# Optimization experiments

Measured on AMD Instinct MI355X. Metric: run time of the kernel, lower is better.

Reference implementation:

```python
import jax, jax.numpy as jnp
import numpy as np

B, C, H, W, K = 4, 64, 128, 128, 3
K2 = K * K
PAD = (K - 1) // 2  # same padding for 3x3


def setup_inputs() -> dict:
    key = jax.random.key(0)
    ks = jax.random.split(key, 9)
    s = 0.05
    return {
        "x": jax.random.normal(ks[0], (B, C, H, W), jnp.float32),
        "inter": jax.random.normal(ks[1], (B, C, H, W), jnp.float32),
        # offset/mask predictor conv: input cat([x, inter]) -> 3*K2 channels (dy, dx, mask)
        "w_offset": jax.random.normal(ks[2], (3 * K2, 2 * C, K, K), jnp.float32) * s,
        "b_offset": jnp.zeros((3 * K2,), jnp.float32),
        # deformable conv weight (bias=False per DGM init)
        "w_dcn": jax.random.normal(ks[3], (C, C, K, K), jnp.float32) * s,
        # SFT gamma branch: two 1x1 convs (bias=False)
        "w_g1": jax.random.normal(ks[4], (C, C), jnp.float32) * s,
        "w_g2": jax.random.normal(ks[5], (C, C), jnp.float32) * s,
        # SFT beta branch: two 1x1 convs (bias=False)
        "w_b1": jax.random.normal(ks[6], (C, C), jnp.float32) * s,
        "w_b2": jax.random.normal(ks[7], (C, C), jnp.float32) * s,
    }


def _lrelu(v):
    # LeakyReLU(0.1)
    return jnp.where(v >= 0, v, 0.1 * v)


def _conv(x, w, b=None):
    y = jax.lax.conv_general_dilated(
        x, w, window_strides=(1, 1), padding=[(PAD, PAD), (PAD, PAD)],
        dimension_numbers=("NCHW", "OIHW", "NCHW"))
    if b is not None:
        y = y + b[None, :, None, None]
    return y


def _bilinear_gather(x, py, px):
    """x: [B,C,H,W]; py, px: [B,K2,H,W] float sample coords.
    Returns samples [B,K2,H,W,C]; out-of-bounds treated as zero (DCN zero-pad)."""
    y0 = jnp.floor(py)
    x0 = jnp.floor(px)
    wy = (py - y0)[..., None]
    wx = (px - x0)[..., None]

    def gather(yi, xi):
        valid = ((yi >= 0) & (yi < H) & (xi >= 0) & (xi < W)).astype(x.dtype)
        yc = jnp.clip(yi, 0, H - 1).astype(jnp.int32)
        xc = jnp.clip(xi, 0, W - 1).astype(jnp.int32)
        bidx = jnp.arange(B)[:, None, None, None]
        v = x[bidx, :, yc, xc]  # advanced indexing -> [B,K2,H,W,C]
        return v * valid[..., None]

    v00 = gather(y0, x0)
    v01 = gather(y0, x0 + 1)
    v10 = gather(y0 + 1, x0)
    v11 = gather(y0 + 1, x0 + 1)
    return (v00 * (1 - wy) * (1 - wx) + v01 * (1 - wy) * wx
            + v10 * wy * (1 - wx) + v11 * wy * wx)


def _dgm_forward(x, inter, w_offset, b_offset, w_dcn, w_g1, w_g2, w_b1, w_b2):
    # --- WADCN branch: modulated deformable conv, offsets predicted from cat(x, inter)
    om = _conv(jnp.concatenate([x, inter], axis=1), w_offset, b_offset)  # [B,3K2,H,W]
    dy, dx, m = jnp.split(om, 3, axis=1)  # each [B,K2,H,W]
    mask = jax.nn.sigmoid(m)

    ky, kx = jnp.meshgrid(jnp.arange(K), jnp.arange(K), indexing="ij")
    ky = ky.reshape(K2).astype(x.dtype)
    kx = kx.reshape(K2).astype(x.dtype)
    hh = jnp.arange(H, dtype=x.dtype)
    ww = jnp.arange(W, dtype=x.dtype)
    # sample coords: base grid + kernel-tap offset + learned offset
    py = hh[None, None, :, None] + (ky - PAD)[None, :, None, None] + dy  # [B,K2,H,W]
    px = ww[None, None, None, :] + (kx - PAD)[None, :, None, None] + dx

    samp = _bilinear_gather(x, py, px) * mask[..., None]  # [B,K2,H,W,C]
    dcn_out = jnp.einsum("bkhwc,ock->bohw", samp, w_dcn.reshape(C, C, K2))

    # --- SFT branch: two 1x1-conv + LeakyReLU chains producing gamma/beta
    gamma = jnp.einsum("oc,bchw->bohw", w_g2,
                       _lrelu(jnp.einsum("oc,bchw->bohw", w_g1, inter)))
    beta = jnp.einsum("oc,bchw->bohw", w_b2,
                      _lrelu(jnp.einsum("oc,bchw->bohw", w_b1, inter)))
    sft_out = x * gamma + beta

    # --- fused residual combine (DGM.relu is defined but never applied)
    return x + dcn_out + sft_out


def reference(x, inter, w_offset, b_offset, w_dcn, w_g1, w_g2, w_b1, w_b2):
    return _dgm_forward(x, inter, w_offset, b_offset, w_dcn, w_g1, w_g2, w_b1, w_b2)
```

## Files before the change

kernel.cpp:

```cpp
#include <hip/hip_runtime.h>
#include <hip/hip_bf16.h>
#include <math.h>

#define BB 4
#define CC 64
#define HH 128
#define WW 128
#define HW (HH*WW)
#define NPIX (BB*HW)

typedef __attribute__((ext_vector_type(8))) short short8;
typedef __attribute__((ext_vector_type(4))) float f32x4;

__device__ __forceinline__ float bf2f(ushort u) {
  union { unsigned u; float f; } v; v.u = ((unsigned)u) << 16; return v.f;
}
__device__ __forceinline__ ushort f2bf(float f) {
  __hip_bfloat16 h = __float2bfloat16(f); return *(ushort*)&h;
}

__global__ __launch_bounds__(256) void k_prep(
    const float* __restrict__ x, const float* __restrict__ inter,
    const float* __restrict__ w_off, const float* __restrict__ w_dcn,
    const float* __restrict__ wg1, const float* __restrict__ wb1,
    const float* __restrict__ wg2, const float* __restrict__ wb2,
    ushort* __restrict__ x_clh, ushort* __restrict__ inter_clh,
    ushort* __restrict__ wfb, ushort* __restrict__ wdT,
    ushort* __restrict__ w1gb, ushort* __restrict__ w1bb,
    ushort* __restrict__ w2gb, ushort* __restrict__ w2bb,
    float* __restrict__ zp) {
  __shared__ __align__(16) float tile[64 * 128];
  int blk = blockIdx.x;
  int tid = threadIdx.x;
  if (blk < 1024) {
    int sel = blk >> 9;
    int bh = blk & 511;
    int b = bh >> 7, h = bh & 127;
    const float* src = sel ? inter : x;
    ushort* dst = sel ? inter_clh : x_clh;
    const float* sp = src + (size_t)(b * 64) * HW + h * WW;
#pragma unroll
    for (int it = 0; it < 8; ++it) {
      int idx = it * 256 + tid;
      int c = idx >> 5, wq = idx & 31;
      float4 v = *(const float4*)(sp + (size_t)c * HW + wq * 4);
      int s = (c >> 3) & 7;
      *(float4*)(&tile[c * 128 + ((wq ^ s) << 2)]) = v;
    }
    __syncthreads();
    ushort* dp = dst + ((size_t)b * HW + h * WW) * 64;
#pragma unroll
    for (int it = 0; it < 4; ++it) {
      int idx = it * 256 + tid;
      int w = idx >> 3, c8 = idx & 7;
      short8 outv;
#pragma unroll
      for (int j = 0; j < 8; ++j) {
        int c = c8 * 8 + j;
        int sl = (w >> 2) ^ c8;
        float f = tile[c * 128 + (sl << 2) + (w & 3)];
        outv[j] = (short)f2bf(f);
      }
      *(short8*)(dp + (size_t)w * 64 + c8 * 8) = outv;
    }
  } else if (blk < 1168) {
    int i = (blk - 1024) * 256 + tid;
    if (i < 64) zp[i] = 0.f;
    if (i < 9 * 32 * 128) {
      int tap = i >> 12, rem = i & 4095, m = rem >> 7, c = rem & 127;
      float v = (m < 27) ? w_off[(size_t)(m * 128 + c) * 9 + tap] : 0.f;
      wfb[i] = f2bf(v);
    }
  } else if (blk < 1312) {
    int i = (blk - 1168) * 256 + tid;
    if (i < 64 * 64 * 9) {
      int o = i / 576, rem = i % 576, k = rem >> 6, c = rem & 63;
      wdT[i] = f2bf(w_dcn[(o * 64 + c) * 9 + k]);
    }
  } else {
    int i = (blk - 1312) * 256 + tid;
    int m = i >> 12, j = i & 4095;
    const float* src = (m == 0) ? wg1 : (m == 1) ? wb1 : (m == 2) ? wg2 : wb2;
    ushort* dst = (m == 0) ? w1gb : (m == 1) ? w1bb : (m == 2) ? w2gb : w2bb;
    dst[j] = f2bf(src[j]);
  }
}

#define CPITCH 72
#define SPITCH 200
#define NPX 32
#define FPX 72

__global__ __launch_bounds__(256) void k_omega(
    const float* __restrict__ x, const ushort* __restrict__ x_clh,
    const ushort* __restrict__ inter_clh,
    const float* __restrict__ b_off, const ushort* __restrict__ wfb,
    const ushort* __restrict__ wdT,
    const ushort* __restrict__ w1gb, const ushort* __restrict__ w1bb,
    const ushort* __restrict__ w2gb, const ushort* __restrict__ w2bb,
    const ushort* __restrict__ zp16, float* __restrict__ out) {
  __shared__ __align__(16) ushort BIGB[6 * 34 * CPITCH];
  ushort* S  = BIGB;
  ushort* Sg = BIGB + 6400;
  ushort* Sb = Sg + NPX * FPX;
  int*   cy  = (int*)(BIGB + 6400);
  int*   cx  = cy + 288;
  float* cwy = (float*)(cx + 288);
  float* cwx = cwy + 288;
  float* cm  = cwx + 288;
  float* oml = (float*)(BIGB + 11008);

  int tid = threadIdx.x;
  int wave = tid >> 6, lane = tid & 63;
  int quad = lane >> 4, col = lane & 15;
  int rr = lane >> 3, g = lane & 7;
  int pg0 = blockIdx.x * NPX;
  int b = pg0 >> 14, hw0 = pg0 & 16383;
  int h = hw0 >> 7, w0 = hw0 & 127;
  int pt = wave >> 1, mt = wave & 1;
  int o_base = __builtin_amdgcn_readfirstlane(wave * 16);

  {
    int ch = (tid & 7) * 8;
    unsigned bbase = (unsigned)b * HW;
#pragma unroll
    for (int it = 0; it < 7; ++it) {
      int e = it * 32 + (tid >> 3);
      if (e < 204) {
        int srcrow = e / 34, pxl = e % 34;
        int src = srcrow / 3, row = srcrow % 3;
        int hs = h + row - 1;
        int ps = w0 + pxl - 1;
        bool ok = ((unsigned)hs < 128u) && ((unsigned)ps < 128u);
        int hc = hs < 0 ? 0 : (hs > 127 ? 127 : hs);
        int pc = ps < 0 ? 0 : (ps > 127 ? 127 : ps);
        const ushort* sb = src ? inter_clh : x_clh;
        short8 v = *(const short8*)(sb + ((size_t)(bbase + (hc << 7) + pc)) * 64 + ch);
        short8 z = {0, 0, 0, 0, 0, 0, 0, 0};
        if (!ok) v = z;
        *(short8*)(&BIGB[e * CPITCH + ch]) = v;
      }
    }
  }
  __syncthreads();

  f32x4 accx = {0.f, 0.f, 0.f, 0.f}, acci = {0.f, 0.f, 0.f, 0.f};
  {
    const ushort* wb0 = wfb + (size_t)(mt * 16 + col) * 128 + quad * 8;
    int pxb = pt * 16 + col;
#pragma unroll
    for (int ky = 0; ky < 3; ++ky) {
#pragma unroll
      for (int kx = 0; kx < 3; ++kx) {
        int tap = ky * 3 + kx;
        const ushort* wt = wb0 + (size_t)tap * 4096;
#pragma unroll
        for (int ks = 0; ks < 2; ++ks) {
          short8 a0 = *(const short8*)(wt + ks * 32);
          short8 b0 = *(const short8*)(&BIGB[(ky * 34 + pxb + kx) * CPITCH + ks * 32 + quad * 8]);
          accx = __builtin_amdgcn_mfma_f32_16x16x32_bf16(a0, b0, accx, 0, 0, 0);
          short8 a1 = *(const short8*)(wt + 64 + ks * 32);
          short8 b1 = *(const short8*)(&BIGB[((3 + ky) * 34 + pxb + kx) * CPITCH + ks * 32 + quad * 8]);
          acci = __builtin_amdgcn_mfma_f32_16x16x32_bf16(a1, b1, acci, 0, 0, 0);
        }
      }
    }
  }
  __syncthreads();

#pragma unroll
  for (int r = 0; r < 4; ++r) {
    int o = mt * 16 + quad * 4 + r;
    if (o < 27) oml[o * 33 + pt * 16 + col] = accx[r] + acci[r];
  }

  f32x4 ag[2], ab[2];
#pragma unroll
  for (int nt = 0; nt < 2; ++nt) {
    ag[nt] = (f32x4){0.f, 0.f, 0.f, 0.f};
    ab[nt] = (f32x4){0.f, 0.f, 0.f, 0.f};
  }
#pragma unroll
  for (int ks = 0; ks < 2; ++ks) {
    short8 a_g = *(const short8*)(w1gb + (size_t)(o_base + col) * 64 + ks * 32 + quad * 8);
    short8 a_b = *(const short8*)(w1bb + (size_t)(o_base + col) * 64 + ks * 32 + quad * 8);
#pragma unroll
    for (int nt = 0; nt < 2; ++nt) {
      short8 bf = *(const short8*)(inter_clh + (size_t)(pg0 + nt * 16 + col) * 64 + ks * 32 + quad * 8);
      ag[nt] = __builtin_amdgcn_mfma_f32_16x16x32_bf16(a_g, bf, ag[nt], 0, 0, 0);
      ab[nt] = __builtin_amdgcn_mfma_f32_16x16x32_bf16(a_b, bf, ab[nt], 0, 0, 0);
    }
  }
#pragma unroll
  for (int nt = 0; nt < 2; ++nt) {
    int px = nt * 16 + col;
    ushort pkg[4], pkb[4];
#pragma unroll
    for (int r = 0; r < 4; ++r) {
      float vg = ag[nt][r]; vg = vg >= 0.f ? vg : 0.1f * vg;
      float vb = ab[nt][r]; vb = vb >= 0.f ? vb : 0.1f * vb;
      pkg[r] = f2bf(vg); pkb[r] = f2bf(vb);
    }
    *(uint2*)(&Sg[px * FPX + o_base + quad * 4]) = *(uint2*)pkg;
    *(uint2*)(&Sb[px * FPX + o_base + quad * 4]) = *(uint2*)pkb;
  }
  __syncthreads();

  f32x4 gg[2], gb[2];
#pragma unroll
  for (int nt = 0; nt < 2; ++nt) {
    gg[nt] = (f32x4){0.f, 0.f, 0.f, 0.f};
    gb[nt] = (f32x4){0.f, 0.f, 0.f, 0.f};
  }
#pragma unroll
  for (int ks = 0; ks < 2; ++ks) {
    short8 a_g = *(const short8*)(w2gb + (size_t)(o_base + col) * 64 + ks * 32 + quad * 8);
    short8 a_b = *(const short8*)(w2bb + (size_t)(o_base + col) * 64 + ks * 32 + quad * 8);
#pragma unroll
    for (int nt = 0; nt < 2; ++nt) {
      short8 bgf = *(const short8*)(Sg + (nt * 16 + col) * FPX + ks * 32 + quad * 8);
      short8 bbf = *(const short8*)(Sb + (nt * 16 + col) * FPX + ks * 32 + quad * 8);
      gg[nt] = __builtin_amdgcn_mfma_f32_16x16x32_bf16(a_g, bgf, gg[nt], 0, 0, 0);
      gb[nt] = __builtin_amdgcn_mfma_f32_16x16x32_bf16(a_b, bbf, gb[nt], 0, 0, 0);
    }
  }
  float xv[2][4];
#pragma unroll
  for (int nt = 0; nt < 2; ++nt)
#pragma unroll
    for (int r = 0; r < 4; ++r) {
      int o = o_base + quad * 4 + r;
      xv[nt][r] = x[(size_t)(b * 64 + o) * HW + hw0 + nt * 16 + col];
    }
  __syncthreads();

  for (int i = tid; i < 9 * NPX; i += 256) {
    int k = i >> 5, p = i & 31;
    float dy = oml[k * 33 + p] + b_off[k];
    float dx = oml[(9 + k) * 33 + p] + b_off[9 + k];
    float mz = oml[(18 + k) * 33 + p] + b_off[18 + k];
    float py = (float)(h + (k / 3) - 1) + dy;
    float px = (float)(w0 + p + (k % 3) - 1) + dx;
    float y0f = floorf(py), x0f = floorf(px);
    cy[i] = (int)y0f;
    cx[i] = (int)x0f;
    cwy[i] = py - y0f;
    cwx[i] = px - x0f;
    cm[i] = 1.f / (1.f + __expf(-mz));
  }

  f32x4 acc[2];
  acc[0] = (f32x4){0.f, 0.f, 0.f, 0.f};
  acc[1] = (f32x4){0.f, 0.f, 0.f, 0.f};

  const ushort* bp = x_clh + (size_t)b * HW * 64;

  for (int chunk = 0; chunk < 3; ++chunk) {
    __syncthreads();
#pragma unroll
    for (int it = 0; it < 3; ++it) {
      int p = wave * 8 + rr;
      int idx = (chunk * 3 + it) * NPX + p;
      int y0 = cy[idx], x0 = cx[idx];
      float wy = cwy[idx], wx = cwx[idx], m = cm[idx];
      bool yok0 = (unsigned)y0 < 128u, yok1 = (unsigned)(y0 + 1) < 128u;
      bool xok0 = (unsigned)x0 < 128u, xok1 = (unsigned)(x0 + 1) < 128u;
      const ushort* r0 = bp + ((size_t)(int)((y0 << 7) + x0)) * 64 + g * 8;
      const ushort* r1 = r0 + (size_t)WW * 64;
      short8 s00 = *(const short8*)((yok0 && xok0) ? r0 : zp16);
      short8 s01 = *(const short8*)((yok0 && xok1) ? (r0 + 64) : zp16);
      short8 s10 = *(const short8*)((yok1 && xok0) ? r1 : zp16);
      short8 s11 = *(const short8*)((yok1 && xok1) ? (r1 + 64) : zp16);
      short8 outv;
#pragma unroll
      for (int j = 0; j < 8; ++j) {
        float v00 = bf2f((ushort)s00[j]), v01 = bf2f((ushort)s01[j]);
        float v10 = bf2f((ushort)s10[j]), v11 = bf2f((ushort)s11[j]);
        float top = v00 + (v01 - v00) * wx;
        float bot = v10 + (v11 - v10) * wx;
        float val = top + (bot - top) * wy;
        outv[j] = (short)f2bf(val * m);
      }
      *(short8*)(&S[p * SPITCH + it * 64 + g * 8]) = outv;
    }
    __syncthreads();
    const ushort* wrow = wdT + (size_t)(o_base + col) * 576 + chunk * 192 + quad * 8;
    const ushort* srow = S + quad * 8;
#pragma unroll
    for (int ks = 0; ks < 6; ++ks) {
      short8 a = *(const short8*)(wrow + ks * 32);
#pragma unroll
      for (int nt = 0; nt < 2; ++nt) {
        short8 bf = *(const short8*)(srow + (nt * 16 + col) * SPITCH + ks * 32);
        acc[nt] = __builtin_amdgcn_mfma_f32_16x16x32_bf16(a, bf, acc[nt], 0, 0, 0);
      }
    }
  }

#pragma unroll
  for (int nt = 0; nt < 2; ++nt) {
#pragma unroll
    for (int r = 0; r < 4; ++r) {
      int o = o_base + quad * 4 + r;
      size_t idx = (size_t)(b * 64 + o) * HW + hw0 + nt * 16 + col;
      out[idx] = xv[nt][r] + xv[nt][r] * gg[nt][r] + gb[nt][r] + acc[nt][r];
    }
  }
}

extern "C" void kernel_launch(void* const* d_in, const int* in_sizes, int n_in,
                              void* d_out, int out_size, void* d_ws, size_t ws_size,
                              hipStream_t stream) {
  const float* x     = (const float*)d_in[0];
  const float* inter = (const float*)d_in[1];
  const float* w_off = (const float*)d_in[2];
  const float* b_off = (const float*)d_in[3];
  const float* w_dcn = (const float*)d_in[4];
  const float* wg1   = (const float*)d_in[5];
  const float* wg2   = (const float*)d_in[6];
  const float* wb1   = (const float*)d_in[7];
  const float* wb2   = (const float*)d_in[8];
  float* out = (float*)d_out;

  float* ws        = (float*)d_ws;
  ushort* x_clh    = (ushort*)ws;
  ushort* inter_clh= (ushort*)(ws + 2097152);
  ushort* wfb      = (ushort*)(ws + 5963776);
  ushort* wdT      = (ushort*)(ws + 5982208);
  ushort* w1gb     = (ushort*)(ws + 6000640);
  ushort* w1bb     = (ushort*)(ws + 6002688);
  ushort* w2gb     = (ushort*)(ws + 6004736);
  ushort* w2bb     = (ushort*)(ws + 6006784);
  float* zp        = ws + 6008832;

  k_prep<<<1376, 256, 0, stream>>>(x, inter, w_off, w_dcn, wg1, wb1, wg2, wb2,
                                   x_clh, inter_clh, wfb, wdT,
                                   w1gb, w1bb, w2gb, w2bb, zp);

  k_omega<<<2048, 256, 0, stream>>>(x, x_clh, inter_clh, b_off, wfb, wdT,
                                    w1gb, w1bb, w2gb, w2bb,
                                    (const ushort*)zp, out);
}
```

Before: 169.6 us.

## Load offset-conv operands from global directly, shrink LDS, raise occupancy

The offset-predictor conv no longer stages a 6x34 halo tile of x/inter in shared memory. Each MFMA B operand is now read straight from the channel-last bf16 global buffers, with a zero page used for out-of-bounds taps. This frees LDS, so the buffer drops to about 19.5KB, packs the y/x coordinates into one int, and reuses oml for the mask, while launch bounds request 8 blocks per CU. The change also drops several barriers, folds the SFT epilogue early to free registers, and swizzles block indices across batches. The cost is redundant global/L2 reads of halo pixels and loop unrolling disabled in places.

New measurement: 212.3 us. 25.2% more time.

```diff
diff --git a/kernel.cpp b/kernel.cpp
--- a/kernel.cpp
+++ b/kernel.cpp
@@ -86,12 +86,11 @@
   }
 }
 
-#define CPITCH 72
-#define SPITCH 200
+#define SPITCH 196
 #define NPX 32
 #define FPX 72
 
-__global__ __launch_bounds__(256) void k_omega(
+__global__ __launch_bounds__(256, 8) void k_omega(
     const float* __restrict__ x, const ushort* __restrict__ x_clh,
     const ushort* __restrict__ inter_clh,
     const float* __restrict__ b_off, const ushort* __restrict__ wfb,
@@ -99,75 +98,57 @@
     const ushort* __restrict__ w1gb, const ushort* __restrict__ w1bb,
     const ushort* __restrict__ w2gb, const ushort* __restrict__ w2bb,
     const ushort* __restrict__ zp16, float* __restrict__ out) {
-  __shared__ __align__(16) ushort BIGB[6 * 34 * CPITCH];
-  ushort* S  = BIGB;
-  ushort* Sg = BIGB + 6400;
-  ushort* Sb = Sg + NPX * FPX;
-  int*   cy  = (int*)(BIGB + 6400);
-  int*   cx  = cy + 288;
-  float* cwy = (float*)(cx + 288);
-  float* cwx = cwy + 288;
-  float* cm  = cwx + 288;
-  float* oml = (float*)(BIGB + 11008);
+  __shared__ __align__(16) ushort LDSB[9792];
+  ushort* S  = LDSB;
+  ushort* Sg = LDSB;
+  ushort* Sb = LDSB + NPX * FPX;
+  int*   cycx = (int*)(LDSB + 6272);
+  float* cwy  = (float*)(LDSB + 6848);
+  float* cwx  = (float*)(LDSB + 7424);
+  float* oml  = (float*)(LDSB + 8000);
 
   int tid = threadIdx.x;
   int wave = tid >> 6, lane = tid & 63;
   int quad = lane >> 4, col = lane & 15;
   int rr = lane >> 3, g = lane & 7;
-  int pg0 = blockIdx.x * NPX;
+  int bid = blockIdx.x;
+  int wid = (bid & 7) * 256 + (bid >> 3);
+  int pg0 = wid * NPX;
   int b = pg0 >> 14, hw0 = pg0 & 16383;
   int h = hw0 >> 7, w0 = hw0 & 127;
   int pt = wave >> 1, mt = wave & 1;
   int o_base = __builtin_amdgcn_readfirstlane(wave * 16);
 
-  {
-    int ch = (tid & 7) * 8;
-    unsigned bbase = (unsigned)b * HW;
-#pragma unroll
-    for (int it = 0; it < 7; ++it) {
-      int e = it * 32 + (tid >> 3);
-      if (e < 204) {
-        int srcrow = e / 34, pxl = e % 34;
-        int src = srcrow / 3, row = srcrow % 3;
-        int hs = h + row - 1;
-        int ps = w0 + pxl - 1;
-        bool ok = ((unsigned)hs < 128u) && ((unsigned)ps < 128u);
-        int hc = hs < 0 ? 0 : (hs > 127 ? 127 : hs);
-        int pc = ps < 0 ? 0 : (ps > 127 ? 127 : ps);
-        const ushort* sb = src ? inter_clh : x_clh;
-        short8 v = *(const short8*)(sb + ((size_t)(bbase + (hc << 7) + pc)) * 64 + ch);
-        short8 z = {0, 0, 0, 0, 0, 0, 0, 0};
-        if (!ok) v = z;
-        *(short8*)(&BIGB[e * CPITCH + ch]) = v;
-      }
-    }
-  }
-  __syncthreads();
-
   f32x4 accx = {0.f, 0.f, 0.f, 0.f}, acci = {0.f, 0.f, 0.f, 0.f};
   {
     const ushort* wb0 = wfb + (size_t)(mt * 16 + col) * 128 + quad * 8;
-    int pxb = pt * 16 + col;
-#pragma unroll
+    int pxcol = pt * 16 + col;
+    unsigned bbase = (unsigned)b * HW;
+#pragma unroll 1
     for (int ky = 0; ky < 3; ++ky) {
+      int hs = h + ky - 1;
+      bool oky = (unsigned)hs < 128u;
+      int rowb = hs << 7;
 #pragma unroll
       for (int kx = 0; kx < 3; ++kx) {
-        int tap = ky * 3 + kx;
-        const ushort* wt = wb0 + (size_t)tap * 4096;
+        int ws = w0 + pxcol + kx - 1;
+        bool ok = oky && ((unsigned)ws < 128u);
+        long long poff = (long long)(int)(bbase + rowb + ws) * 64;
+        const ushort* bx = (ok ? x_clh + poff : zp16) + quad * 8;
+        const ushort* bi = (ok ? inter_clh + poff : zp16) + quad * 8;
+        const ushort* wt = wb0 + (size_t)(ky * 3 + kx) * 4096;
 #pragma unroll
         for (int ks = 0; ks < 2; ++ks) {
           short8 a0 = *(const short8*)(wt + ks * 32);
-          short8 b0 = *(const short8*)(&BIGB[(ky * 34 + pxb + kx) * CPITCH + ks * 32 + quad * 8]);
+          short8 b0 = *(const short8*)(bx + ks * 32);
           accx = __builtin_amdgcn_mfma_f32_16x16x32_bf16(a0, b0, accx, 0, 0, 0);
           short8 a1 = *(const short8*)(wt + 64 + ks * 32);
-          short8 b1 = *(const short8*)(&BIGB[((3 + ky) * 34 + pxb + kx) * CPITCH + ks * 32 + quad * 8]);
+          short8 b1 = *(const short8*)(bi + ks * 32);
           acci = __builtin_amdgcn_mfma_f32_16x16x32_bf16(a1, b1, acci, 0, 0, 0);
         }
       }
     }
   }
-  __syncthreads();
-
 #pragma unroll
   for (int r = 0; r < 4; ++r) {
     int o = mt * 16 + quad * 4 + r;
@@ -224,15 +205,15 @@
       gb[nt] = __builtin_amdgcn_mfma_f32_16x16x32_bf16(a_b, bbf, gb[nt], 0, 0, 0);
     }
   }
-  float xv[2][4];
+  float ev[2][4];
 #pragma unroll
   for (int nt = 0; nt < 2; ++nt)
 #pragma unroll
     for (int r = 0; r < 4; ++r) {
       int o = o_base + quad * 4 + r;
-      xv[nt][r] = x[(size_t)(b * 64 + o) * HW + hw0 + nt * 16 + col];
-    }
-  __syncthreads();
+      float xv = x[(size_t)(b * 64 + o) * HW + hw0 + nt * 16 + col];
+      ev[nt][r] = xv + xv * gg[nt][r] + gb[nt][r];
+    }
 
   for (int i = tid; i < 9 * NPX; i += 256) {
     int k = i >> 5, p = i & 31;
@@ -242,11 +223,11 @@
     float py = (float)(h + (k / 3) - 1) + dy;
     float px = (float)(w0 + p + (k % 3) - 1) + dx;
     float y0f = floorf(py), x0f = floorf(px);
-    cy[i] = (int)y0f;
-    cx[i] = (int)x0f;
+    int iy = (int)y0f, ix = (int)x0f;
+    cycx[i] = (iy & 0xffff) | (ix << 16);
     cwy[i] = py - y0f;
     cwx[i] = px - x0f;
-    cm[i] = 1.f / (1.f + __expf(-mz));
+    oml[(18 + k) * 33 + p] = 1.f / (1.f + __expf(-mz));
   }
 
   f32x4 acc[2];
@@ -254,15 +235,20 @@
   acc[1] = (f32x4){0.f, 0.f, 0.f, 0.f};
 
   const ushort* bp = x_clh + (size_t)b * HW * 64;
-
+  int p = wave * 8 + rr;
+
+#pragma unroll 1
   for (int chunk = 0; chunk < 3; ++chunk) {
     __syncthreads();
-#pragma unroll
+#pragma unroll 1
     for (int it = 0; it < 3; ++it) {
-      int p = wave * 8 + rr;
-      int idx = (chunk * 3 + it) * NPX + p;
-      int y0 = cy[idx], x0 = cx[idx];
-      float wy = cwy[idx], wx = cwx[idx], m = cm[idx];
+      int k = chunk * 3 + it;
+      int idx = k * 32 + p;
+      int v = cycx[idx];
+      int y0 = (int)(short)(v & 0xffff);
+      int x0 = v >> 16;
+      float wy = cwy[idx], wx = cwx[idx];
+      float m = oml[(18 + k) * 33 + p];
       bool yok0 = (unsigned)y0 < 128u, yok1 = (unsigned)(y0 + 1) < 128u;
       bool xok0 = (unsigned)x0 < 128u, xok1 = (unsigned)(x0 + 1) < 128u;
       const ushort* r0 = bp + ((size_t)(int)((y0 << 7) + x0)) * 64 + g * 8;
@@ -303,7 +289,7 @@
     for (int r = 0; r < 4; ++r) {
       int o = o_base + quad * 4 + r;
       size_t idx = (size_t)(b * 64 + o) * HW + hw0 + nt * 16 + col;
-      out[idx] = xv[nt][r] + xv[nt][r] * gg[nt][r] + gb[nt][r] + acc[nt][r];
+      out[idx] = ev[nt][r] + acc[nt][r];
     }
   }
 }
```

## Prefetch next chunk's bilinear gather loads into registers before the MFMA stage

Applied to the files above, without the earlier changes.

Software-pipelines the deformable sampling: the four bilinear corner loads for the next chunk of taps are issued into registers before the MFMA accumulation of the current chunk, so global gather latency overlaps with compute. It also folds the SFT epilogue (x + x*gamma + beta) into a single value early, which frees registers, and compacts the workspace layout. The cost is higher register pressure from holding twelve short8 values per thread, which can lower occupancy.

Measured after the change: 174.2 us. +2.7%, slower.

```diff
diff --git a/kernel.cpp b/kernel.cpp
--- a/kernel.cpp
+++ b/kernel.cpp
@@ -224,13 +224,14 @@
       gb[nt] = __builtin_amdgcn_mfma_f32_16x16x32_bf16(a_b, bbf, gb[nt], 0, 0, 0);
     }
   }
-  float xv[2][4];
+  float ev[2][4];
 #pragma unroll
   for (int nt = 0; nt < 2; ++nt)
 #pragma unroll
     for (int r = 0; r < 4; ++r) {
       int o = o_base + quad * 4 + r;
-      xv[nt][r] = x[(size_t)(b * 64 + o) * HW + hw0 + nt * 16 + col];
+      float xv = x[(size_t)(b * 64 + o) * HW + hw0 + nt * 16 + col];
+      ev[nt][r] = xv + xv * gg[nt][r] + gb[nt][r];
     }
   __syncthreads();
 
@@ -254,28 +255,39 @@
   acc[1] = (f32x4){0.f, 0.f, 0.f, 0.f};
 
   const ushort* bp = x_clh + (size_t)b * HW * 64;
-
+  int p = wave * 8 + rr;
+
+  short8 k00[3], k01[3], k10[3], k11[3];
+  float kwy[3], kwx[3], km[3];
+
+  __syncthreads();
+
+#pragma unroll
+  for (int it = 0; it < 3; ++it) {
+    int idx = it * NPX + p;
+    int y0 = cy[idx], x0 = cx[idx];
+    kwy[it] = cwy[idx]; kwx[it] = cwx[idx]; km[it] = cm[idx];
+    bool yok0 = (unsigned)y0 < 128u, yok1 = (unsigned)(y0 + 1) < 128u;
+    bool xok0 = (unsigned)x0 < 128u, xok1 = (unsigned)(x0 + 1) < 128u;
+    const ushort* r0 = bp + ((size_t)(int)((y0 << 7) + x0)) * 64 + g * 8;
+    const ushort* r1 = r0 + (size_t)WW * 64;
+    k00[it] = *(const short8*)((yok0 && xok0) ? r0 : zp16);
+    k01[it] = *(const short8*)((yok0 && xok1) ? (r0 + 64) : zp16);
+    k10[it] = *(const short8*)((yok1 && xok0) ? r1 : zp16);
+    k11[it] = *(const short8*)((yok1 && xok1) ? (r1 + 64) : zp16);
+  }
+
+#pragma unroll 1
   for (int chunk = 0; chunk < 3; ++chunk) {
-    __syncthreads();
+    if (chunk) __syncthreads();
 #pragma unroll
     for (int it = 0; it < 3; ++it) {
-      int p = wave * 8 + rr;
-      int idx = (chunk * 3 + it) * NPX + p;
-      int y0 = cy[idx], x0 = cx[idx];
-      float wy = cwy[idx], wx = cwx[idx], m = cm[idx];
-      bool yok0 = (unsigned)y0 < 128u, yok1 = (unsigned)(y0 + 1) < 128u;
-      bool xok0 = (unsigned)x0 < 128u, xok1 = (unsigned)(x0 + 1) < 128u;
-      const ushort* r0 = bp + ((size_t)(int)((y0 << 7) + x0)) * 64 + g * 8;
-      const ushort* r1 = r0 + (size_t)WW * 64;
-      short8 s00 = *(const short8*)((yok0 && xok0) ? r0 : zp16);
-      short8 s01 = *(const short8*)((yok0 && xok1) ? (r0 + 64) : zp16);
-      short8 s10 = *(const short8*)((yok1 && xok0) ? r1 : zp16);
-      short8 s11 = *(const short8*)((yok1 && xok1) ? (r1 + 64) : zp16);
+      float wy = kwy[it], wx = kwx[it], m = km[it];
       short8 outv;
 #pragma unroll
       for (int j = 0; j < 8; ++j) {
-        float v00 = bf2f((ushort)s00[j]), v01 = bf2f((ushort)s01[j]);
-        float v10 = bf2f((ushort)s10[j]), v11 = bf2f((ushort)s11[j]);
+        float v00 = bf2f((ushort)k00[it][j]), v01 = bf2f((ushort)k01[it][j]);
+        float v10 = bf2f((ushort)k10[it][j]), v11 = bf2f((ushort)k11[it][j]);
         float top = v00 + (v01 - v00) * wx;
         float bot = v10 + (v11 - v10) * wx;
         float val = top + (bot - top) * wy;
@@ -283,6 +295,22 @@
       }
       *(short8*)(&S[p * SPITCH + it * 64 + g * 8]) = outv;
     }
+    if (chunk < 2) {
+#pragma unroll
+      for (int it = 0; it < 3; ++it) {
+        int idx = ((chunk + 1) * 3 + it) * NPX + p;
+        int y0 = cy[idx], x0 = cx[idx];
+        kwy[it] = cwy[idx]; kwx[it] = cwx[idx]; km[it] = cm[idx];
+        bool yok0 = (unsigned)y0 < 128u, yok1 = (unsigned)(y0 + 1) < 128u;
+        bool xok0 = (unsigned)x0 < 128u, xok1 = (unsigned)(x0 + 1) < 128u;
+        const ushort* r0 = bp + ((size_t)(int)((y0 << 7) + x0)) * 64 + g * 8;
+        const ushort* r1 = r0 + (size_t)WW * 64;
+        k00[it] = *(const short8*)((yok0 && xok0) ? r0 : zp16);
+        k01[it] = *(const short8*)((yok0 && xok1) ? (r0 + 64) : zp16);
+        k10[it] = *(const short8*)((yok1 && xok0) ? r1 : zp16);
+        k11[it] = *(const short8*)((yok1 && xok1) ? (r1 + 64) : zp16);
+      }
+    }
     __syncthreads();
     const ushort* wrow = wdT + (size_t)(o_base + col) * 576 + chunk * 192 + quad * 8;
     const ushort* srow = S + quad * 8;
@@ -303,7 +331,7 @@
     for (int r = 0; r < 4; ++r) {
       int o = o_base + quad * 4 + r;
       size_t idx = (size_t)(b * 64 + o) * HW + hw0 + nt * 16 + col;
-      out[idx] = xv[nt][r] + xv[nt][r] * gg[nt][r] + gb[nt][r] + acc[nt][r];
+      out[idx] = ev[nt][r] + acc[nt][r];
     }
   }
 }
@@ -325,13 +353,13 @@
   float* ws        = (float*)d_ws;
   ushort* x_clh    = (ushort*)ws;
   ushort* inter_clh= (ushort*)(ws + 2097152);
-  ushort* wfb      = (ushort*)(ws + 5963776);
-  ushort* wdT      = (ushort*)(ws + 5982208);
-  ushort* w1gb     = (ushort*)(ws + 6000640);
-  ushort* w1bb     = (ushort*)(ws + 6002688);
-  ushort* w2gb     = (ushort*)(ws + 6004736);
-  ushort* w2bb     = (ushort*)(ws + 6006784);
-  float* zp        = ws + 6008832;
+  ushort* wfb      = (ushort*)(ws + 4194304);
+  ushort* wdT      = (ushort*)(ws + 4212736);
+  ushort* w1gb     = (ushort*)(ws + 4231168);
+  ushort* w1bb     = (ushort*)(ws + 4233216);
+  ushort* w2gb     = (ushort*)(ws + 4235264);
+  ushort* w2bb     = (ushort*)(ws + 4237312);
+  float* zp        = ws + 4239360;
 
   k_prep<<<1376, 256, 0, stream>>>(x, inter, w_off, w_dcn, wg1, wb1, wg2, wb2,
                                    x_clh, inter_clh, wfb, wdT,
```
